# Performance work log

Hardware: AMD Instinct MI355X
Metric: run time of the kernel (lower is better)

The kernel has to match this reference:

```python
import jax, jax.numpy as jnp
import numpy as np

C = 1.0                 # ball curvature magnitude (k = -c)
SQRT_C = float(np.sqrt(C))
MIN_NORM = 1e-15
BALL_EPS = 4e-3         # geoopt float32 projection eps


def _artanh(x):
    return jnp.arctanh(jnp.clip(x, -1.0 + 1e-7, 1.0 - 1e-7))


def _norm(x):
    return jnp.clip(jnp.linalg.norm(x, axis=-1, keepdims=True), MIN_NORM)


def expmap0(u):
    n = _norm(u)
    return jnp.tanh(SQRT_C * n) * u / (SQRT_C * n)


def logmap0(y):
    n = _norm(y)
    return _artanh(SQRT_C * n) * y / (SQRT_C * n)


def mobius_add(x, y):
    x2 = jnp.sum(x * x, axis=-1, keepdims=True)
    y2 = jnp.sum(y * y, axis=-1, keepdims=True)
    xy = jnp.sum(x * y, axis=-1, keepdims=True)
    num = (1.0 + 2.0 * C * xy + C * y2) * x + (1.0 - C * x2) * y
    den = 1.0 + 2.0 * C * xy + C * C * x2 * y2
    return num / jnp.clip(den, MIN_NORM)


def mobius_matvec(W, x):
    # x: [N, in], W: [out, in]
    mx = x @ W.T                                   # [N, out]
    xn = _norm(x)
    mxn = _norm(mx)
    res = jnp.tanh(mxn / xn * _artanh(SQRT_C * xn)) * mx / (mxn * SQRT_C)
    zero = jnp.linalg.norm(mx, axis=-1, keepdims=True) <= 1e-10
    return jnp.where(zero, jnp.zeros_like(res), res)


def project(x):
    n = _norm(x)
    maxnorm = (1.0 - BALL_EPS) / SQRT_C
    return jnp.where(n > maxnorm, x * (maxnorm / n), x)


def setup_inputs() -> dict:
    key = jax.random.key(0)
    k1, k2, k3, k4, k5 = jax.random.split(key, 5)
    N, E, D_IN, D_OUT = 100000, 600000, 128, 128
    x_h = jax.random.normal(k1, (N, D_IN), dtype=jnp.float32) * 0.05  # inside ball
    edge_index = jax.random.randint(k2, (2, E), 0, N, dtype=jnp.int64)
    edge_weight = jax.random.uniform(k3, (E,), dtype=jnp.float32)
    xav = float(np.sqrt(2.0 / (D_IN + D_OUT)))
    W = jax.random.normal(k4, (D_OUT, D_IN), dtype=jnp.float32) * xav
    b = jax.random.normal(k5, (D_OUT,), dtype=jnp.float32) * 0.01
    a = jnp.asarray(0.25, dtype=jnp.float32)  # PReLU slope
    return {"x_h": x_h, "edge_index": edge_index, "edge_weight": edge_weight,
            "W": W, "b": b, "a": a}


def reference(x_h, edge_index, edge_weight, W, b, a):
    N = x_h.shape[0]
    # HyperbolicLinear: mobius matvec + mobius bias add
    h = mobius_matvec(W, x_h)
    h = mobius_add(h, expmap0(b))
    # tangent-space aggregation
    h_t = logmap0(h)                                  # [N, D]
    src, dst = edge_index[0], edge_index[1]
    msg = h_t[src] * edge_weight[:, None]             # [E, D]
    agg = jax.ops.segment_sum(msg, dst, num_segments=N) + h_t
    # mobius PReLU activation
    h2_t = logmap0(expmap0(agg))
    h2_t = jnp.where(h2_t >= 0, h2_t, a * h2_t)
    return project(expmap0(h2_t))
```

## Files before the change

kernel.cpp:

```cpp
#include <hip/hip_runtime.h>
#include <hip/hip_fp16.h>
#include <cstdint>

#define D 128
#define BLK 256

constexpr float MINN    = 1e-15f;
constexpr float ATCLIP  = 1.0f - 1e-7f;
constexpr float BALLEPS = 4e-3f;

typedef _Float16 f16x8 __attribute__((ext_vector_type(8)));
typedef float    f32x4 __attribute__((ext_vector_type(4)));

union H4 { _Float16 h[4]; uint2 u2; };
union H8 { _Float16 h[8]; uint4 u4; };

typedef __attribute__((address_space(1))) const void gas_v;
typedef __attribute__((address_space(3))) void las_v;

__device__ __forceinline__ float red64(float v) {
    v += __shfl_xor(v, 1, 64);
    v += __shfl_xor(v, 2, 64);
    v += __shfl_xor(v, 4, 64);
    v += __shfl_xor(v, 8, 64);
    v += __shfl_xor(v, 16, 64);
    v += __shfl_xor(v, 32, 64);
    return v;
}

__device__ __forceinline__ float red16(float v) {
    v += __shfl_xor(v, 1, 64);
    v += __shfl_xor(v, 2, 64);
    v += __shfl_xor(v, 4, 64);
    v += __shfl_xor(v, 8, 64);
    return v;
}

__device__ __forceinline__ float tanh_fast(float x) {
    float e = __expf(2.f * fminf(x, 15.f));
    return __fdividef(e - 1.f, e + 1.f);
}
__device__ __forceinline__ float artanh_fast(float x) {
    x = fminf(x, ATCLIP);
    return 0.5f * __logf(__fdividef(1.f + x, 1.f - x));
}

__global__ void k_wcvt(const float* __restrict__ W, _Float16* __restrict__ Wh) {
    int i = blockIdx.x * 256 + threadIdx.x;
    if (i >= 2048) return;
    int f = i >> 7;
    int r = i & 127;
    const float4* src = (const float4*)(W + r * 128 + f * 8);
    float4 v0 = src[0], v1 = src[1];
    H8 u;
    u.h[0] = (_Float16)v0.x; u.h[1] = (_Float16)v0.y;
    u.h[2] = (_Float16)v0.z; u.h[3] = (_Float16)v0.w;
    u.h[4] = (_Float16)v1.x; u.h[5] = (_Float16)v1.y;
    u.h[6] = (_Float16)v1.z; u.h[7] = (_Float16)v1.w;
    *(uint4*)(Wh + i * 8) = u.u4;
}

__global__ __launch_bounds__(BLK) void k_node_mfma(
    const float* __restrict__ x, const _Float16* __restrict__ Wh,
    const float* __restrict__ b, uint2* __restrict__ ht, int N,
    const int* __restrict__ ei, int* __restrict__ cnt, int E, int eslice)
{
    __shared__ float xs[64 * 128];
    __shared__ float ps[D];

    const int t     = threadIdx.x;
    const int node0 = blockIdx.x * 64;
    const int lane  = t & 63;
    const int w     = t >> 6;

#pragma unroll
    for (int i = 0; i < 8; ++i) {
        int P      = (w * 8 + i) * 64 + lane;
        int node   = P >> 5;
        int q      = (P & 31) ^ (node & 7);
        int node_g = min(node0 + node, N - 1);
        const float* src = x + (size_t)node_g * 128 + q * 4;
        char* dst = (char*)xs + (size_t)(w * 8 + i) * 1024;
        __builtin_amdgcn_global_load_lds((gas_v*)src, (las_v*)dst, 16, 0, 0);
    }

    {
        int e0 = blockIdx.x * eslice;
        for (int i = t; i < eslice; i += BLK) {
            int e = e0 + i;
            if (e < E) atomicAdd(&cnt[ei[E + e]], 1);
        }
    }

    float2 b2 = ((const float2*)b)[lane];
    float pb  = fmaf(b2.x, b2.x, b2.y * b2.y);
    float bn2 = red64(pb);
    float bnc    = fmaxf(sqrtf(bn2), MINN);
    float bscale = __fdividef(tanh_fast(bnc), bnc);
    if (t < D) ps[t] = b[t] * bscale;
    const float y2 = bscale * bscale * bn2;
    __syncthreads();

    const int c = lane & 15;
    const int g = lane >> 4;

    f32x4 Cf[8];
#pragma unroll
    for (int mt = 0; mt < 8; ++mt) Cf[mt] = (f32x4){0.f, 0.f, 0.f, 0.f};

    const int bnode = w * 16 + c;
    const int sw    = bnode & 7;
    const float* xrow = &xs[bnode * 128];
    float px = 0.f;

#pragma unroll
    for (int s = 0; s < 4; ++s) {
        int q0 = s * 8 + g * 2;
        f32x4 lo = *(const f32x4*)&xrow[(q0 ^ sw) * 4];
        f32x4 hi = *(const f32x4*)&xrow[((q0 + 1) ^ sw) * 4];
        px = fmaf(lo[0], lo[0], px); px = fmaf(lo[1], lo[1], px);
        px = fmaf(lo[2], lo[2], px); px = fmaf(lo[3], lo[3], px);
        px = fmaf(hi[0], hi[0], px); px = fmaf(hi[1], hi[1], px);
        px = fmaf(hi[2], hi[2], px); px = fmaf(hi[3], hi[3], px);
        f16x8 Bf;
        Bf[0] = (_Float16)lo[0]; Bf[1] = (_Float16)lo[1];
        Bf[2] = (_Float16)lo[2]; Bf[3] = (_Float16)lo[3];
        Bf[4] = (_Float16)hi[0]; Bf[5] = (_Float16)hi[1];
        Bf[6] = (_Float16)hi[2]; Bf[7] = (_Float16)hi[3];
        const _Float16* wp = Wh + ((s * 4 + g) << 10) + (c << 3);
#pragma unroll
        for (int mt = 0; mt < 8; ++mt) {
            f16x8 Af = *(const f16x8*)&wp[mt << 7];
            Cf[mt] = __builtin_amdgcn_mfma_f32_16x16x32_f16(Af, Bf, Cf[mt], 0, 0, 0);
        }
    }

    float pm = 0.f, pd = 0.f;
    const float4* ps4 = (const float4*)ps;
#pragma unroll
    for (int mt = 0; mt < 8; ++mt) {
        float4 pv = ps4[mt * 4 + g];
        pm = fmaf(Cf[mt][0], Cf[mt][0], pm);
        pm = fmaf(Cf[mt][1], Cf[mt][1], pm);
        pm = fmaf(Cf[mt][2], Cf[mt][2], pm);
        pm = fmaf(Cf[mt][3], Cf[mt][3], pm);
        pd = fmaf(Cf[mt][0], pv.x, pd);
        pd = fmaf(Cf[mt][1], pv.y, pd);
        pd = fmaf(Cf[mt][2], pv.z, pd);
        pd = fmaf(Cf[mt][3], pv.w, pd);
    }
    float xn2 = px;
    xn2 += __shfl_xor(xn2, 16); xn2 += __shfl_xor(xn2, 32);
    pm  += __shfl_xor(pm, 16);  pm  += __shfl_xor(pm, 32);
    pd  += __shfl_xor(pd, 16);  pd  += __shfl_xor(pd, 32);

    float xn      = fmaxf(sqrtf(xn2), MINN);
    float mxn_raw = sqrtf(pm);
    float mxn     = fmaxf(mxn_raw, MINN);
    float alpha   = __fdividef(tanh_fast(__fdividef(mxn, xn) * artanh_fast(xn)), mxn);
    if (mxn_raw <= 1e-10f) alpha = 0.f;

    float x2  = alpha * alpha * pm;
    float xy  = alpha * pd;
    float den = fmaxf(fmaf(x2, y2, 1.f + 2.f * xy), MINN);
    float ca  = __fdividef((1.f + 2.f * xy + y2) * alpha, den);
    float cb  = __fdividef(1.f - x2, den);

    float hn2 = ca * ca * pm + 2.f * ca * cb * pd + cb * cb * y2;
    float hn  = fmaxf(sqrtf(hn2), MINN);
    float lsc = __fdividef(artanh_fast(hn), hn);
    float s1  = lsc * ca, s2 = lsc * cb;

    uint2* lout = (uint2*)((char*)xs + (size_t)w * 8192);
#pragma unroll
    for (int mt = 0; mt < 8; ++mt) {
        float4 pv = ps4[mt * 4 + g];
        H4 u;
        u.h[0] = (_Float16)fmaf(s1, Cf[mt][0], s2 * pv.x);
        u.h[1] = (_Float16)fmaf(s1, Cf[mt][1], s2 * pv.y);
        u.h[2] = (_Float16)fmaf(s1, Cf[mt][2], s2 * pv.z);
        u.h[3] = (_Float16)fmaf(s1, Cf[mt][3], s2 * pv.w);
        lout[c * 33 + mt * 4 + g] = u.u2;
    }
    __syncthreads();

    for (int it = 0; it < 8; ++it) {
        int lin  = it * BLK + t;
        int node = lin >> 5;
        int col  = lin & 31;
        int gn   = node0 + node;
        if (gn < N) {
            const uint2* lsrc = (const uint2*)((const char*)xs + (size_t)(node >> 4) * 8192);
            ht[(size_t)gn * 32 + col] = lsrc[(node & 15) * 33 + col];
        }
    }
}

__global__ __launch_bounds__(256) void k_scan1(
    const int* __restrict__ cnt, int* __restrict__ ptr,
    int* __restrict__ part, int N)
{
    __shared__ int s[256];
    int t = threadIdx.x;
    int base = blockIdx.x * 1024 + t * 4;
    int v0 = 0, v1 = 0, v2 = 0, v3 = 0;
    if (base + 3 < N) {
        int4 q = *(const int4*)&cnt[base];
        v0 = q.x; v1 = q.y; v2 = q.z; v3 = q.w;
    } else {
        if (base + 0 < N) v0 = cnt[base + 0];
        if (base + 1 < N) v1 = cnt[base + 1];
        if (base + 2 < N) v2 = cnt[base + 2];
        if (base + 3 < N) v3 = cnt[base + 3];
    }
    int sum = v0 + v1 + v2 + v3;
    s[t] = sum;
    __syncthreads();
    for (int off = 1; off < 256; off <<= 1) {
        int xv = (t >= off) ? s[t - off] : 0;
        __syncthreads();
        s[t] += xv;
        __syncthreads();
    }
    int excl = s[t] - sum;
    if (t == 255) part[blockIdx.x] = s[255];
    int r = excl;
    if (base + 0 < N) ptr[base + 0] = r; r += v0;
    if (base + 1 < N) ptr[base + 1] = r; r += v1;
    if (base + 2 < N) ptr[base + 2] = r; r += v2;
    if (base + 3 < N) ptr[base + 3] = r;
}

__global__ __launch_bounds__(256) void k_scan2(int* __restrict__ part, int nc) {
    __shared__ int s[256];
    int t = threadIdx.x;
    int v = (t < nc) ? part[t] : 0;
    s[t] = v;
    __syncthreads();
    for (int off = 1; off < 256; off <<= 1) {
        int xv = (t >= off) ? s[t - off] : 0;
        __syncthreads();
        s[t] += xv;
        __syncthreads();
    }
    if (t < nc) part[t] = s[t] - v;
}

__global__ void k_scatter(const int* __restrict__ ei, const float* __restrict__ ew,
                          int* __restrict__ ptr, const int* __restrict__ part,
                          int2* __restrict__ sorted, int E)
{
    int e = blockIdx.x * 256 + threadIdx.x;
    if (e >= E) return;
    int src = ei[e];
    int dst = ei[E + e];
    float w = ew[e];
    int pos = atomicAdd(&ptr[dst], 1) + part[dst >> 10];
    sorted[pos] = make_int2(src << 8, __float_as_int(w));
}

__global__ __launch_bounds__(256) void k_agg_final(
    const char* __restrict__ htb, const int* __restrict__ ptr,
    const int* __restrict__ part, const int2* __restrict__ sorted,
    const float* __restrict__ a_in, float* __restrict__ out, int N)
{
    const int t   = threadIdx.x;
    const int li  = t & 15;
    const int grp = t >> 4;
    const int n   = blockIdx.x * 16 + grp;
    if (n >= N) return;
    const float a = a_in[0];

    H8 own; own.u4 = *(const uint4*)(htb + (size_t)n * 256 + li * 16);
    float acc[8];
#pragma unroll
    for (int k = 0; k < 8; ++k) acc[k] = (float)own.h[k];

    int s0 = (n > 0) ? (ptr[n - 1] + part[(n - 1) >> 10]) : 0;
    int e0 = ptr[n] + part[n >> 10];

    const int lioff = li * 16;
    int j = s0;
    for (; j + 2 <= e0; j += 2) {
        int2 d0 = sorted[j];
        int2 d1 = sorted[j + 1];
        H8 g0, g1;
        g0.u4 = *(const uint4*)(htb + (unsigned)d0.x + lioff);
        g1.u4 = *(const uint4*)(htb + (unsigned)d1.x + lioff);
        float w0 = __int_as_float(d0.y);
        float w1 = __int_as_float(d1.y);
#pragma unroll
        for (int k = 0; k < 8; ++k) acc[k] = fmaf((float)g0.h[k], w0, acc[k]);
#pragma unroll
        for (int k = 0; k < 8; ++k) acc[k] = fmaf((float)g1.h[k], w1, acc[k]);
    }
    if (j < e0) {
        int2 d = sorted[j];
        H8 g; g.u4 = *(const uint4*)(htb + (unsigned)d.x + lioff);
        float w = __int_as_float(d.y);
#pragma unroll
        for (int k = 0; k < 8; ++k) acc[k] = fmaf((float)g.h[k], w, acc[k]);
    }

    float pv = 0.f;
#pragma unroll
    for (int k = 0; k < 8; ++k) {
        float v = acc[k];
        v = (v >= 0.f) ? v : a * v;
        acc[k] = v;
        pv = fmaf(v, v, pv);
    }
    float m2 = red16(pv);
    float rc = fmaxf(sqrtf(m2), MINN);
    float te = tanh_fast(rc);
    const float maxn = 1.0f - BALLEPS;
    float fsc = __fdividef(fminf(fmaxf(te, MINN), maxn), rc);

    float4 o0 = make_float4(fsc * acc[0], fsc * acc[1], fsc * acc[2], fsc * acc[3]);
    float4 o1 = make_float4(fsc * acc[4], fsc * acc[5], fsc * acc[6], fsc * acc[7]);
    float4* orow = (float4*)(out + (size_t)n * D);
    orow[li * 2 + 0] = o0;
    orow[li * 2 + 1] = o1;
}

extern "C" void kernel_launch(void* const* d_in, const int* in_sizes, int n_in,
                              void* d_out, int out_size, void* d_ws, size_t ws_size,
                              hipStream_t stream)
{
    const float* x  = (const float*)d_in[0];
    const int*   ei = (const int*)  d_in[1];
    const float* ew = (const float*)d_in[2];
    const float* W  = (const float*)d_in[3];
    const float* b  = (const float*)d_in[4];
    const float* a  = (const float*)d_in[5];
    float* out = (float*)d_out;

    const int N = in_sizes[0] / D;
    const int E = in_sizes[1] / 2;

    char* ws = (char*)d_ws;
    size_t HT_B    = (size_t)N * D * 2;
    uint2*     ht     = (uint2*)ws;
    int*       cnt    = (int*)(ws + HT_B);
    int*       ptr    = (int*)(ws + HT_B + (size_t)N * 4);
    int*       part   = (int*)(ws + HT_B + (size_t)N * 8);
    int2*      sorted = (int2*)(ws + HT_B + (size_t)N * 8 + 1024);
    _Float16*  Wh     = (_Float16*)(ws + HT_B + (size_t)N * 8 + 1024 + (size_t)E * 8);

    int nc  = (N + 1023) / 1024;
    int nb1 = (N + 63) / 64;
    int eslice = (E + nb1 - 1) / nb1;

    hipMemsetAsync(cnt, 0, (size_t)N * 4, stream);
    k_wcvt<<<8, 256, 0, stream>>>(W, Wh);
    k_node_mfma<<<nb1, BLK, 0, stream>>>(x, Wh, b, ht, N, ei, cnt, E, eslice);
    k_scan1<<<nc, 256, 0, stream>>>(cnt, ptr, part, N);
    k_scan2<<<1, 256, 0, stream>>>(part, nc);
    k_scatter<<<(E + 255) / 256, 256, 0, stream>>>(ei, ew, ptr, part, sorted, E);
    k_agg_final<<<(N + 15) / 16, 256, 0, stream>>>((const char*)ht, ptr, part, sorted, a, out, N);
}
```

Before: 228.6 us.

## Record per-edge ranks during counting to drop scatter atomics; fuse memset into prep kernel

The degree-count atomics now return each edge's slot index, stored in a rank buffer, so the scatter pass computes positions without a second round of atomics. This path is used only when the workspace is large enough; otherwise the old atomic scatter runs. The counting loop moves to the end of the node kernel, after the feature stores. The cnt memset is folded into the W-conversion kernel, and the scaled-bias shared array is replaced by direct bias loads with the scale factored out. Segment bounds in aggregation now come from cnt. The change trades an extra E-sized int write and read for removing contended atomics in the scatter.

Measured after the change: 191.9 us. 1.19x faster.

```diff
diff --git a/kernel.cpp b/kernel.cpp
--- a/kernel.cpp
+++ b/kernel.cpp
@@ -45,28 +45,42 @@
     return 0.5f * __logf(__fdividef(1.f + x, 1.f - x));
 }
 
-__global__ void k_wcvt(const float* __restrict__ W, _Float16* __restrict__ Wh) {
-    int i = blockIdx.x * 256 + threadIdx.x;
-    if (i >= 2048) return;
-    int f = i >> 7;
-    int r = i & 127;
-    const float4* src = (const float4*)(W + r * 128 + f * 8);
-    float4 v0 = src[0], v1 = src[1];
-    H8 u;
-    u.h[0] = (_Float16)v0.x; u.h[1] = (_Float16)v0.y;
-    u.h[2] = (_Float16)v0.z; u.h[3] = (_Float16)v0.w;
-    u.h[4] = (_Float16)v1.x; u.h[5] = (_Float16)v1.y;
-    u.h[6] = (_Float16)v1.z; u.h[7] = (_Float16)v1.w;
-    *(uint4*)(Wh + i * 8) = u.u4;
+__global__ __launch_bounds__(256) void k_prep(const float* __restrict__ W,
+                                              _Float16* __restrict__ Wh,
+                                              int* __restrict__ cnt, int N)
+{
+    const int t = threadIdx.x;
+    const int bid = blockIdx.x;
+    if (bid < 8) {
+        int i = bid * 256 + t;
+        int f = i >> 7;
+        int r = i & 127;
+        const float4* src = (const float4*)(W + r * 128 + f * 8);
+        float4 v0 = src[0], v1 = src[1];
+        H8 u;
+        u.h[0] = (_Float16)v0.x; u.h[1] = (_Float16)v0.y;
+        u.h[2] = (_Float16)v0.z; u.h[3] = (_Float16)v0.w;
+        u.h[4] = (_Float16)v1.x; u.h[5] = (_Float16)v1.y;
+        u.h[6] = (_Float16)v1.z; u.h[7] = (_Float16)v1.w;
+        *(uint4*)(Wh + i * 8) = u.u4;
+    } else {
+        int i = (bid - 8) * 256 + t;
+        int base = i * 4;
+        if (base + 3 < N) {
+            *(int4*)(cnt + base) = make_int4(0, 0, 0, 0);
+        } else if (base < N) {
+            for (int k = base; k < N; ++k) cnt[k] = 0;
+        }
+    }
 }
 
 __global__ __launch_bounds__(BLK) void k_node_mfma(
     const float* __restrict__ x, const _Float16* __restrict__ Wh,
     const float* __restrict__ b, uint2* __restrict__ ht, int N,
-    const int* __restrict__ ei, int* __restrict__ cnt, int E, int eslice)
+    const int* __restrict__ ei, int* __restrict__ cnt,
+    int* __restrict__ rank, int E, int eslice, int use_rank)
 {
     __shared__ float xs[64 * 128];
-    __shared__ float ps[D];
 
     const int t     = threadIdx.x;
     const int node0 = blockIdx.x * 64;
@@ -84,20 +98,11 @@
         __builtin_amdgcn_global_load_lds((gas_v*)src, (las_v*)dst, 16, 0, 0);
     }
 
-    {
-        int e0 = blockIdx.x * eslice;
-        for (int i = t; i < eslice; i += BLK) {
-            int e = e0 + i;
-            if (e < E) atomicAdd(&cnt[ei[E + e]], 1);
-        }
-    }
-
     float2 b2 = ((const float2*)b)[lane];
     float pb  = fmaf(b2.x, b2.x, b2.y * b2.y);
     float bn2 = red64(pb);
     float bnc    = fmaxf(sqrtf(bn2), MINN);
     float bscale = __fdividef(tanh_fast(bnc), bnc);
-    if (t < D) ps[t] = b[t] * bscale;
     const float y2 = bscale * bscale * bn2;
     __syncthreads();
 
@@ -135,24 +140,25 @@
         }
     }
 
-    float pm = 0.f, pd = 0.f;
-    const float4* ps4 = (const float4*)ps;
+    const float4* b4 = (const float4*)b;
+    float pm = 0.f, pdb = 0.f;
 #pragma unroll
     for (int mt = 0; mt < 8; ++mt) {
-        float4 pv = ps4[mt * 4 + g];
-        pm = fmaf(Cf[mt][0], Cf[mt][0], pm);
-        pm = fmaf(Cf[mt][1], Cf[mt][1], pm);
-        pm = fmaf(Cf[mt][2], Cf[mt][2], pm);
-        pm = fmaf(Cf[mt][3], Cf[mt][3], pm);
-        pd = fmaf(Cf[mt][0], pv.x, pd);
-        pd = fmaf(Cf[mt][1], pv.y, pd);
-        pd = fmaf(Cf[mt][2], pv.z, pd);
-        pd = fmaf(Cf[mt][3], pv.w, pd);
+        float4 bv = b4[mt * 4 + g];
+        pm  = fmaf(Cf[mt][0], Cf[mt][0], pm);
+        pm  = fmaf(Cf[mt][1], Cf[mt][1], pm);
+        pm  = fmaf(Cf[mt][2], Cf[mt][2], pm);
+        pm  = fmaf(Cf[mt][3], Cf[mt][3], pm);
+        pdb = fmaf(Cf[mt][0], bv.x, pdb);
+        pdb = fmaf(Cf[mt][1], bv.y, pdb);
+        pdb = fmaf(Cf[mt][2], bv.z, pdb);
+        pdb = fmaf(Cf[mt][3], bv.w, pdb);
     }
     float xn2 = px;
     xn2 += __shfl_xor(xn2, 16); xn2 += __shfl_xor(xn2, 32);
     pm  += __shfl_xor(pm, 16);  pm  += __shfl_xor(pm, 32);
-    pd  += __shfl_xor(pd, 16);  pd  += __shfl_xor(pd, 32);
+    pdb += __shfl_xor(pdb, 16); pdb += __shfl_xor(pdb, 32);
+    float pd = bscale * pdb;
 
     float xn      = fmaxf(sqrtf(xn2), MINN);
     float mxn_raw = sqrtf(pm);
@@ -169,17 +175,18 @@
     float hn2 = ca * ca * pm + 2.f * ca * cb * pd + cb * cb * y2;
     float hn  = fmaxf(sqrtf(hn2), MINN);
     float lsc = __fdividef(artanh_fast(hn), hn);
-    float s1  = lsc * ca, s2 = lsc * cb;
+    float s1  = lsc * ca;
+    float s2b = lsc * cb * bscale;
 
     uint2* lout = (uint2*)((char*)xs + (size_t)w * 8192);
 #pragma unroll
     for (int mt = 0; mt < 8; ++mt) {
-        float4 pv = ps4[mt * 4 + g];
+        float4 bv = b4[mt * 4 + g];
         H4 u;
-        u.h[0] = (_Float16)fmaf(s1, Cf[mt][0], s2 * pv.x);
-        u.h[1] = (_Float16)fmaf(s1, Cf[mt][1], s2 * pv.y);
-        u.h[2] = (_Float16)fmaf(s1, Cf[mt][2], s2 * pv.z);
-        u.h[3] = (_Float16)fmaf(s1, Cf[mt][3], s2 * pv.w);
+        u.h[0] = (_Float16)fmaf(s1, Cf[mt][0], s2b * bv.x);
+        u.h[1] = (_Float16)fmaf(s1, Cf[mt][1], s2b * bv.y);
+        u.h[2] = (_Float16)fmaf(s1, Cf[mt][2], s2b * bv.z);
+        u.h[3] = (_Float16)fmaf(s1, Cf[mt][3], s2b * bv.w);
         lout[c * 33 + mt * 4 + g] = u.u2;
     }
     __syncthreads();
@@ -192,6 +199,21 @@
         if (gn < N) {
             const uint2* lsrc = (const uint2*)((const char*)xs + (size_t)(node >> 4) * 8192);
             ht[(size_t)gn * 32 + col] = lsrc[(node & 15) * 33 + col];
+        }
+    }
+
+    {
+        int e0 = blockIdx.x * eslice;
+        if (use_rank) {
+            for (int i = t; i < eslice; i += BLK) {
+                int e = e0 + i;
+                if (e < E) rank[e] = atomicAdd(&cnt[ei[E + e]], 1);
+            }
+        } else {
+            for (int i = t; i < eslice; i += BLK) {
+                int e = e0 + i;
+                if (e < E) atomicAdd(&cnt[ei[E + e]], 1);
+            }
         }
     }
 }
@@ -246,9 +268,24 @@
     if (t < nc) part[t] = s[t] - v;
 }
 
-__global__ void k_scatter(const int* __restrict__ ei, const float* __restrict__ ew,
-                          int* __restrict__ ptr, const int* __restrict__ part,
-                          int2* __restrict__ sorted, int E)
+__global__ __launch_bounds__(256) void k_scatter_rank(
+    const int* __restrict__ ei, const float* __restrict__ ew,
+    const int* __restrict__ ptr, const int* __restrict__ part,
+    const int* __restrict__ rank, int2* __restrict__ sorted, int E)
+{
+    int e = blockIdx.x * 256 + threadIdx.x;
+    if (e >= E) return;
+    int src = ei[e];
+    int dst = ei[E + e];
+    float w = ew[e];
+    int pos = ptr[dst] + part[dst >> 10] + rank[e];
+    sorted[pos] = make_int2(src << 8, __float_as_int(w));
+}
+
+__global__ __launch_bounds__(256) void k_scatter_atomic(
+    const int* __restrict__ ei, const float* __restrict__ ew,
+    int* __restrict__ ptr, const int* __restrict__ part,
+    int2* __restrict__ sorted, int E)
 {
     int e = blockIdx.x * 256 + threadIdx.x;
     if (e >= E) return;
@@ -261,8 +298,9 @@
 
 __global__ __launch_bounds__(256) void k_agg_final(
     const char* __restrict__ htb, const int* __restrict__ ptr,
-    const int* __restrict__ part, const int2* __restrict__ sorted,
-    const float* __restrict__ a_in, float* __restrict__ out, int N)
+    const int* __restrict__ part, const int* __restrict__ cnt,
+    const int2* __restrict__ sorted, const float* __restrict__ a_in,
+    float* __restrict__ out, int N, int rmode)
 {
     const int t   = threadIdx.x;
     const int li  = t & 15;
@@ -276,8 +314,10 @@
 #pragma unroll
     for (int k = 0; k < 8; ++k) acc[k] = (float)own.h[k];
 
-    int s0 = (n > 0) ? (ptr[n - 1] + part[(n - 1) >> 10]) : 0;
-    int e0 = ptr[n] + part[n >> 10];
+    int basep = ptr[n] + part[n >> 10];
+    int cn    = cnt[n];
+    int s0    = rmode ? basep : basep - cn;
+    int e0    = s0 + cn;
 
     const int lioff = li * 16;
     int j = s0;
@@ -346,16 +386,23 @@
     int*       part   = (int*)(ws + HT_B + (size_t)N * 8);
     int2*      sorted = (int2*)(ws + HT_B + (size_t)N * 8 + 1024);
     _Float16*  Wh     = (_Float16*)(ws + HT_B + (size_t)N * 8 + 1024 + (size_t)E * 8);
+    size_t base_end   = HT_B + (size_t)N * 8 + 1024 + (size_t)E * 8 + 32768;
+    int*       rank   = (int*)(ws + base_end);
+    int use_rank = (ws_size >= base_end + (size_t)E * 4) ? 1 : 0;
 
     int nc  = (N + 1023) / 1024;
     int nb1 = (N + 63) / 64;
     int eslice = (E + nb1 - 1) / nb1;
-
-    hipMemsetAsync(cnt, 0, (size_t)N * 4, stream);
-    k_wcvt<<<8, 256, 0, stream>>>(W, Wh);
-    k_node_mfma<<<nb1, BLK, 0, stream>>>(x, Wh, b, ht, N, ei, cnt, E, eslice);
+    int zb  = (((N + 3) / 4) + 255) / 256;
+
+    k_prep<<<8 + zb, 256, 0, stream>>>(W, Wh, cnt, N);
+    k_node_mfma<<<nb1, BLK, 0, stream>>>(x, Wh, b, ht, N, ei, cnt,
+                                         use_rank ? rank : nullptr, E, eslice, use_rank);
     k_scan1<<<nc, 256, 0, stream>>>(cnt, ptr, part, N);
     k_scan2<<<1, 256, 0, stream>>>(part, nc);
-    k_scatter<<<(E + 255) / 256, 256, 0, stream>>>(ei, ew, ptr, part, sorted, E);
-    k_agg_final<<<(N + 15) / 16, 256, 0, stream>>>((const char*)ht, ptr, part, sorted, a, out, N);
-}
+    if (use_rank)
+        k_scatter_rank<<<(E + 255) / 256, 256, 0, stream>>>(ei, ew, ptr, part, rank, sorted, E);
+    else
+        k_scatter_atomic<<<(E + 255) / 256, 256, 0, stream>>>(ei, ew, ptr, part, sorted, E);
+    k_agg_final<<<(N + 15) / 16, 256, 0, stream>>>((const char*)ht, ptr, part, cnt, sorted, a, out, N, use_rank);
+}
```
